# Kernel tuning notes

Measured on AMD Instinct MI355X. Metric: run time of the kernel, lower is better.

The kernel has to match this reference:

```python
import jax, jax.numpy as jnp
import numpy as np

BS, SEQ, D_MODEL = 4, 1024, 4096
N_Q_HEADS, N_KV_HEADS, D_K, D_V = 32, 8, 128, 128
ROPE_BASE = 10000.0


def _rotate_half(x):
    x1, x2 = jnp.split(x, 2, axis=-1)
    return jnp.concatenate([-x2, x1], axis=-1)


def _apply_rope(x, pos0):
    # x: [bs, heads, seq, d]; positions pos0 .. pos0+seq-1
    d = x.shape[-1]
    seq = x.shape[2]
    inv_freq = 1.0 / (ROPE_BASE ** (jnp.arange(0, d, 2, dtype=jnp.float32) / d))  # [d/2]
    pos = (pos0 + jnp.arange(seq)).astype(jnp.float32)  # [seq]
    ang = pos[:, None] * inv_freq[None, :]  # [seq, d/2]
    cos = jnp.concatenate([jnp.cos(ang), jnp.cos(ang)], axis=-1)  # [seq, d]
    sin = jnp.concatenate([jnp.sin(ang), jnp.sin(ang)], axis=-1)
    return x * cos[None, None] + _rotate_half(x) * sin[None, None]


def setup_inputs() -> dict:
    key = jax.random.key(0)
    ks = jax.random.split(key, 8)
    w_scale = 0.02  # keep logits in a sane range (original uses raw normal init)
    return {
        "query": jax.random.normal(ks[0], (BS, SEQ, D_MODEL), dtype=jnp.float32),
        "key": jax.random.normal(ks[1], (BS, SEQ, D_MODEL), dtype=jnp.float32),
        "value": jax.random.normal(ks[2], (BS, SEQ, D_MODEL), dtype=jnp.float32),
        "mask": jnp.zeros((BS, SEQ, SEQ), dtype=jnp.float32),
        "wq": jax.random.normal(ks[3], (D_MODEL, N_Q_HEADS * D_K), dtype=jnp.float32) * w_scale,
        "wk": jax.random.normal(ks[4], (D_MODEL, N_KV_HEADS * D_K), dtype=jnp.float32) * w_scale,
        "wv": jax.random.normal(ks[5], (D_MODEL, N_KV_HEADS * D_V), dtype=jnp.float32) * w_scale,
        "wo": jax.random.normal(ks[6], (N_Q_HEADS * D_V, D_MODEL), dtype=jnp.float32) * w_scale,
        "curr_seq_pos": 0,
    }


def reference(query, key, value, mask, wq, wk, wv, wo, curr_seq_pos):
    bs, sq, _ = query.shape
    n_groups = N_Q_HEADS // N_KV_HEADS
    # projections -> [bs, heads, seq, d]
    q = (query @ wq).reshape(bs, sq, N_Q_HEADS, D_K).transpose((0, 2, 1, 3))
    sk = key.shape[1]
    k = (key @ wk).reshape(bs, sk, N_KV_HEADS, 1, D_K)
    k = jnp.repeat(k, n_groups, axis=3).reshape(bs, sk, N_Q_HEADS, D_K).transpose((0, 2, 1, 3))
    v = (value @ wv).reshape(bs, sk, N_KV_HEADS, 1, D_V)
    v = jnp.repeat(v, n_groups, axis=3).reshape(bs, sk, N_Q_HEADS, D_V).transpose((0, 2, 1, 3))
    scale = jnp.sqrt(jnp.float32(D_K))
    q = _apply_rope(q, curr_seq_pos)
    k = _apply_rope(k, curr_seq_pos)
    # [bs, h, sq, sk]
    raw = jnp.einsum("bhqd,bhkd->bhqk", q, k) / scale
    masked = raw + mask[:bs, None, curr_seq_pos:curr_seq_pos + sq, :sk]
    attn = jax.nn.softmax(masked, axis=-1)
    out = jnp.einsum("bhqk,bhkd->bhqd", attn, v)
    out = out.transpose((0, 2, 1, 3)).reshape(bs, sq, N_Q_HEADS * D_V)
    return out @ wo
```

## Files before the change

kernel.cpp:

```cpp
#include <hip/hip_runtime.h>


using ushort = unsigned short;
typedef __attribute__((ext_vector_type(8))) short short8;
typedef __attribute__((ext_vector_type(4))) short short4v;
typedef __attribute__((ext_vector_type(4))) float f32x4;
typedef __attribute__((ext_vector_type(4))) unsigned int uint4v;

__device__ __forceinline__ ushort f2bf(float x) {
  unsigned int u = __float_as_uint(x);
  u += 0x7FFFu + ((u >> 16) & 1u);
  return (ushort)(u >> 16);
}
__device__ __forceinline__ float bf2f(ushort h) {
  return __uint_as_float(((unsigned int)h) << 16);
}
__device__ __forceinline__ unsigned int cvt_pk_bf16(float lo, float hi) {
  unsigned int r;
  asm("v_cvt_pk_bf16_f32 %0, %1, %2" : "=v"(r) : "v"(lo), "v"(hi));
  return r;
}

__device__ __forceinline__ void async_copy16(const void* g, void* l) {
  __builtin_amdgcn_global_load_lds((const __attribute__((address_space(1))) void*)g,
                                   (__attribute__((address_space(3))) void*)l, 16, 0, 0);
}

__global__ __launch_bounds__(256)
void cvt_f32_bf16(const float* __restrict__ in, ushort* __restrict__ out, int n4) {
  const int i = blockIdx.x * 256 + threadIdx.x;
  if (i < n4) {
    const float4 f = ((const float4*)in)[i];
    short4v v;
    v[0] = (short)f2bf(f.x); v[1] = (short)f2bf(f.y);
    v[2] = (short)f2bf(f.z); v[3] = (short)f2bf(f.w);
    ((short4v*)out)[i] = v;
  }
}

__global__ __launch_bounds__(256)
void transpose_cvt(const float* __restrict__ B, ushort* __restrict__ Bt, int N) {
  __shared__ ushort t[64][72];
  const int n0 = blockIdx.x * 64, k0 = blockIdx.y * 64;
  const int tid = threadIdx.x;
  const int r = tid >> 3, c8 = (tid & 7) * 8;
#pragma unroll
  for (int p = 0; p < 2; p++) {
    const float* src = B + (size_t)(k0 + r + p * 32) * N + n0 + c8;
    const float4 f0 = *(const float4*)src;
    const float4 f1 = *(const float4*)(src + 4);
    ushort* d = &t[r + p * 32][c8];
    d[0] = f2bf(f0.x); d[1] = f2bf(f0.y); d[2] = f2bf(f0.z); d[3] = f2bf(f0.w);
    d[4] = f2bf(f1.x); d[5] = f2bf(f1.y); d[6] = f2bf(f1.z); d[7] = f2bf(f1.w);
  }
  __syncthreads();
#pragma unroll
  for (int p = 0; p < 2; p++) {
    const int n = r + p * 32;
    short8 o;
#pragma unroll
    for (int j = 0; j < 8; j++) o[j] = (short)t[c8 + j][n];
    *(short8*)(Bt + (size_t)(n0 + n) * 4096 + k0 + c8) = o;
  }
}

template <int MODE, bool AF32>
__global__ __launch_bounds__(256, 2)
void gemm_bt(const float* __restrict__ Af, const float* __restrict__ A2f,
             const ushort* __restrict__ Abf, const ushort* __restrict__ Bt,
             ushort* __restrict__ C, ushort* __restrict__ C2,
             float* __restrict__ Cf, const int* __restrict__ posp,
             int N, float scale) {
  constexpr int K = 4096;
  __shared__ alignas(16) ushort As[2][128 * 32];
  __shared__ alignas(16) ushort Bs[2][128 * 32];
  const int tid = threadIdx.x;
  const int wave = tid >> 6, lane = tid & 63;
  const int quad = lane >> 4, l16 = lane & 15;
  const int m0 = blockIdx.y * 128, n0 = blockIdx.x * 128;
  const int wm = (wave & 1) * 64, wn2 = (wave >> 1) * 32;

  const size_t aoff = (size_t)(m0 + wave * 16 + (lane >> 2)) * K + (lane & 3) * 8;
  const float* gAf = nullptr;
  const ushort* gAb = nullptr;
  if constexpr (AF32) {
    const float* Ause = Af;
    if constexpr (MODE == 4) {
      if (n0 >= 1024) Ause = A2f;
    }
    gAf = Ause + aoff;
  } else {
    gAb = Abf + aoff;
  }
  const ushort* gB = Bt + (size_t)(n0 + wave * 16 + (lane >> 2)) * K + (lane & 3) * 8;
  const int woff = wave * 512;
  constexpr size_t rstep = (size_t)64 * K;

  f32x4 acc[4][4] = {};

  if constexpr (AF32) {
    const float4 a0 = *(const float4*)(gAf);
    const float4 a1 = *(const float4*)(gAf + 4);
    const float4 b0 = *(const float4*)(gAf + rstep);
    const float4 b1 = *(const float4*)(gAf + rstep + 4);
    uint4v v0, v1;
    v0[0] = cvt_pk_bf16(a0.x, a0.y); v0[1] = cvt_pk_bf16(a0.z, a0.w);
    v0[2] = cvt_pk_bf16(a1.x, a1.y); v0[3] = cvt_pk_bf16(a1.z, a1.w);
    v1[0] = cvt_pk_bf16(b0.x, b0.y); v1[1] = cvt_pk_bf16(b0.z, b0.w);
    v1[2] = cvt_pk_bf16(b1.x, b1.y); v1[3] = cvt_pk_bf16(b1.z, b1.w);
    *(uint4v*)(As[0] + woff + lane * 8) = v0;
    *(uint4v*)(As[0] + 2048 + woff + lane * 8) = v1;
  } else {
    async_copy16(gAb, As[0] + woff);
    async_copy16(gAb + rstep, As[0] + 2048 + woff);
  }
  async_copy16(gB, Bs[0] + woff);
  async_copy16(gB + rstep, Bs[0] + 2048 + woff);

  for (int kt = 0; kt < K; kt += 32) {
    const int cur = (kt >> 5) & 1;
    const int nxt = cur ^ 1;
    const bool pf = (kt + 32) < K;
    __syncthreads();

    float4 a0, a1, b0, b1;
    if constexpr (AF32) {
      if (pf) {
        a0 = *(const float4*)(gAf + kt + 32);
        a1 = *(const float4*)(gAf + kt + 36);
        b0 = *(const float4*)(gAf + rstep + kt + 32);
        b1 = *(const float4*)(gAf + rstep + kt + 36);
      }
    } else {
      if (pf) {
        async_copy16(gAb + kt + 32, As[nxt] + woff);
        async_copy16(gAb + rstep + kt + 32, As[nxt] + 2048 + woff);
      }
    }
    if (pf) {
      async_copy16(gB + kt + 32, Bs[nxt] + woff);
      async_copy16(gB + rstep + kt + 32, Bs[nxt] + 2048 + woff);
    }

    short8 af[4], bfrag[4];
#pragma unroll
    for (int i = 0; i < 4; i++) {
      af[i] = *(const short8*)(As[cur] + (wm + i * 16 + l16) * 32 + quad * 8);
      bfrag[i] = *(const short8*)(
          Bs[cur] + (wn2 + (i & 1) * 16 + (i >> 1) * 64 + l16) * 32 + quad * 8);
    }
    __builtin_amdgcn_s_setprio(1);
#pragma unroll
    for (int i = 0; i < 4; i++)
#pragma unroll
      for (int j = 0; j < 4; j++)
        acc[i][j] = __builtin_amdgcn_mfma_f32_16x16x32_bf16(af[i], bfrag[j],
                                                            acc[i][j], 0, 0, 0);
    __builtin_amdgcn_s_setprio(0);

    if constexpr (AF32) {
      if (pf) {
        uint4v v0, v1;
        v0[0] = cvt_pk_bf16(a0.x, a0.y); v0[1] = cvt_pk_bf16(a0.z, a0.w);
        v0[2] = cvt_pk_bf16(a1.x, a1.y); v0[3] = cvt_pk_bf16(a1.z, a1.w);
        v1[0] = cvt_pk_bf16(b0.x, b0.y); v1[1] = cvt_pk_bf16(b0.z, b0.w);
        v1[2] = cvt_pk_bf16(b1.x, b1.y); v1[3] = cvt_pk_bf16(b1.z, b1.w);
        *(uint4v*)(As[nxt] + woff + lane * 8) = v0;
        *(uint4v*)(As[nxt] + 2048 + woff + lane * 8) = v1;
      }
    }
  }

  if constexpr (MODE == 0) {
#pragma unroll
    for (int i = 0; i < 4; i++)
#pragma unroll
      for (int j = 0; j < 4; j++) {
        const int n = n0 + wn2 + (j & 1) * 16 + (j >> 1) * 64 + l16;
        const int mb = m0 + wm + i * 16 + quad * 4;
#pragma unroll
        for (int r = 0; r < 4; r++)
          Cf[(size_t)(mb + r) * N + n] = acc[i][j][r] * scale;
      }
  } else {
    const bool kv_v = (MODE == 4) && (n0 >= 1024);
    if (!kv_v) {
      const int pos0 = posp[0];
      const int h = (MODE == 1) ? (n0 >> 7) : (n0 >> 7);
      const int NH = (MODE == 1) ? 32 : 8;
      constexpr float lgbase = -0.20762050593045983f;
      float invf[2];
      invf[0] = exp2f((float)(wn2 + l16) * lgbase);
      invf[1] = exp2f((float)(wn2 + 16 + l16) * lgbase);
#pragma unroll
      for (int i = 0; i < 4; i++) {
#pragma unroll
        for (int r = 0; r < 4; r++) {
          const int m = m0 + wm + i * 16 + quad * 4 + r;
          const int s = m & 1023, bb = m >> 10;
          const float p = (float)(s + pos0);
          ushort* row = C + (((size_t)bb * NH + h) * 1024 + s) * 128;
#pragma unroll
          for (int jj = 0; jj < 2; jj++) {
            float sn, cs;
            sincosf(p * invf[jj], &sn, &cs);
            const float x1 = acc[i][jj][r] * scale;
            const float x2 = acc[i][jj + 2][r] * scale;
            const int dlo = wn2 + jj * 16 + l16;
            row[dlo] = f2bf(x1 * cs - x2 * sn);
            row[dlo + 64] = f2bf(x2 * cs + x1 * sn);
          }
        }
      }
    } else {
      const int hh = (n0 - 1024) >> 7;
#pragma unroll
      for (int i = 0; i < 4; i++)
#pragma unroll
        for (int j = 0; j < 4; j++) {
          const int d = wn2 + (j & 1) * 16 + (j >> 1) * 64 + l16;
          const int mb = m0 + wm + i * 16 + quad * 4;
#pragma unroll
          for (int r = 0; r < 4; r++) {
            const int m = mb + r;
            const int bb = m >> 10, s = m & 1023;
            C2[(((size_t)bb * 8 + hh) * 128 + d) * 1024 + s] = f2bf(acc[i][j][r]);
          }
        }
    }
  }
}

__global__ __launch_bounds__(256, 2)
void attn_kernel(const ushort* __restrict__ Qh, const ushort* __restrict__ Kh,
                 const ushort* __restrict__ Vt, const ushort* __restrict__ Mk,
                 ushort* __restrict__ Oh) {
  __shared__ alignas(16) ushort smem[36864];
  ushort* const Ks0 = smem;
  ushort* const Ks1 = smem + 8192;
  ushort* const Vs0 = smem + 16384;
  ushort* const Vs1 = smem + 24576;
  ushort* const Ps = smem + 32768;
  ushort* const Qtmp = smem + 16384;

  int bid = (blockIdx.z * 32 + blockIdx.y) * 16 + blockIdx.x;
  bid = (bid & 7) * 256 + (bid >> 3);
  const int b = bid >> 9, h = (bid >> 4) & 31;
  const int q0 = (bid & 15) * 64;
  const int hkv = h >> 2;
  const int tid = threadIdx.x;
  const int wave = tid >> 6, lane = tid & 63;
  const int quad = lane >> 4, l16 = lane & 15;
  const int vr = lane >> 3;
  const int vkc = (lane & 7) ^ (vr & 7);

  const ushort* Qg = Qh + (((size_t)b * 32 + h) * 1024 + q0) * 128;
  const ushort* Kg = Kh + ((size_t)b * 8 + hkv) * (size_t)(1024 * 128);
  const ushort* Vg = Vt + ((size_t)b * 8 + hkv) * (size_t)(128 * 1024);
  const ushort* Mg = Mk + ((size_t)b * 1024 + q0) * 1024;

#pragma unroll
  for (int c = 0; c < 4; c++) {
    const int i = wave * 4 + c;
    const int row = i * 4 + quad;
    const int kc = l16 ^ (c * 4 + quad);
    async_copy16(Qg + (size_t)row * 128 + kc * 8, Qtmp + i * 512);
  }
#pragma unroll
  for (int c = 0; c < 4; c++) {
    const int i = wave * 4 + c;
    const int row = i * 4 + quad;
    const int kc = l16 ^ (c * 4 + quad);
    async_copy16(Kg + (size_t)row * 128 + kc * 8, Ks0 + i * 512);
  }
  __asm__ volatile("s_waitcnt vmcnt(0)" ::: "memory");
  short8 qreg[4];
#pragma unroll
  for (int ks = 0; ks < 4; ks++)
    qreg[ks] = *(const short8*)(Qtmp + (size_t)(wave * 16 + l16) * 128 +
                                (((ks * 4 + quad) ^ l16) * 8));
  __syncthreads();
#pragma unroll
  for (int c = 0; c < 4; c++) {
    const int i = wave * 4 + c;
    async_copy16(Vg + (size_t)(i * 8 + vr) * 1024 + vkc * 8, Vs0 + i * 512);
  }

  float m_i[4], l_p[4];
#pragma unroll
  for (int r = 0; r < 4; r++) { m_i[r] = -1e30f; l_p[r] = 0.0f; }
  f32x4 acc[8] = {};

  ushort* const PW = Ps + wave * 1024;

  for (int kt = 0; kt < 1024; kt += 64) {
    const int it = kt >> 6;
    ushort* const Kc = (it & 1) ? Ks1 : Ks0;
    ushort* const Vc = (it & 1) ? Vs1 : Vs0;
    ushort* const Kn = (it & 1) ? Ks0 : Ks1;
    ushort* const Vn = (it & 1) ? Vs0 : Vs1;
    __syncthreads();

    ushort mr[4][4];
#pragma unroll
    for (int nt = 0; nt < 4; nt++)
#pragma unroll
      for (int r = 0; r < 4; r++)
        mr[nt][r] = Mg[(size_t)(wave * 16 + quad * 4 + r) * 1024 +
                       kt + nt * 16 + l16];

    f32x4 s[4] = {};
    __builtin_amdgcn_s_setprio(1);
#pragma unroll
    for (int ks = 0; ks < 4; ks++) {
      const int ko = ((ks * 4 + quad) ^ l16) * 8;
#pragma unroll
      for (int nt = 0; nt < 4; nt++) {
        const short8 bk = *(const short8*)(Kc + (size_t)(nt * 16 + l16) * 128 + ko);
        s[nt] = __builtin_amdgcn_mfma_f32_16x16x32_bf16(qreg[ks], bk, s[nt], 0, 0, 0);
      }
    }
    __builtin_amdgcn_s_setprio(0);

    if (kt < 960) {
#pragma unroll
      for (int c = 0; c < 4; c++) {
        const int i = wave * 4 + c;
        const int row = i * 4 + quad;
        const int kc = l16 ^ (c * 4 + quad);
        async_copy16(Kg + (size_t)(kt + 64 + row) * 128 + kc * 8, Kn + i * 512);
      }
#pragma unroll
      for (int c = 0; c < 4; c++) {
        const int i = wave * 4 + c;
        async_copy16(Vg + (size_t)(i * 8 + vr) * 1024 + kt + 64 + vkc * 8, Vn + i * 512);
      }
    }

#pragma unroll
    for (int nt = 0; nt < 4; nt++)
#pragma unroll
      for (int r = 0; r < 4; r++) s[nt][r] += bf2f(mr[nt][r]);

    float mx[4];
    int need = 0;
#pragma unroll
    for (int r = 0; r < 4; r++) {
      float v = fmaxf(fmaxf(s[0][r], s[1][r]), fmaxf(s[2][r], s[3][r]));
#pragma unroll
      for (int off = 1; off < 16; off <<= 1) v = fmaxf(v, __shfl_xor(v, off));
      mx[r] = v;
      need |= (v > m_i[r] + 8.0f) ? 1 : 0;
    }
    if (__any(need)) {
#pragma unroll
      for (int r = 0; r < 4; r++) {
        const float mnew = fmaxf(m_i[r], mx[r]);
        const float al = __expf(m_i[r] - mnew);
        m_i[r] = mnew;
        l_p[r] *= al;
#pragma unroll
        for (int dt = 0; dt < 8; dt++) acc[dt][r] *= al;
      }
    }

#pragma unroll
    for (int r = 0; r < 4; r++) {
      const int prow = quad * 4 + r;
      const int key8 = ((prow >> 1) & 7) * 8;
      const float p0 = __expf(s[0][r] - m_i[r]);
      const float p1 = __expf(s[1][r] - m_i[r]);
      const float p2 = __expf(s[2][r] - m_i[r]);
      const float p3 = __expf(s[3][r] - m_i[r]);
      l_p[r] += (p0 + p1) + (p2 + p3);
      const unsigned int u01 = cvt_pk_bf16(p0, p1);
      const unsigned int u23 = cvt_pk_bf16(p2, p3);
      ushort* row = PW + prow * 64;
      row[l16 ^ key8] = (ushort)u01;
      row[(16 + l16) ^ key8] = (ushort)(u01 >> 16);
      row[(32 + l16) ^ key8] = (ushort)u23;
      row[(48 + l16) ^ key8] = (ushort)(u23 >> 16);
    }
    __asm__ volatile("s_waitcnt lgkmcnt(0)" ::: "memory");

    __builtin_amdgcn_s_setprio(1);
#pragma unroll
    for (int kk = 0; kk < 2; kk++) {
      const int pslot = ((kk * 4 + quad) ^ (l16 >> 1)) * 8;
      const short8 ap = *(const short8*)(PW + (size_t)l16 * 64 + pslot);
#pragma unroll
      for (int dt = 0; dt < 8; dt++) {
        const int vo = ((kk * 4 + quad) ^ (l16 & 7)) * 8;
        const short8 bv = *(const short8*)(Vc + (size_t)(dt * 16 + l16) * 64 + vo);
        acc[dt] = __builtin_amdgcn_mfma_f32_16x16x32_bf16(ap, bv, acc[dt], 0, 0, 0);
      }
    }
    __builtin_amdgcn_s_setprio(0);
  }

  ushort* Og = Oh + ((size_t)b * 1024 + q0 + wave * 16) * 4096 + h * 128;
#pragma unroll
  for (int r = 0; r < 4; r++) {
    float l = l_p[r];
#pragma unroll
    for (int off = 1; off < 16; off <<= 1) l += __shfl_xor(l, off);
    const float inv = 1.0f / l;
#pragma unroll
    for (int dt = 0; dt < 8; dt++)
      Og[(size_t)(quad * 4 + r) * 4096 + dt * 16 + l16] = f2bf(acc[dt][r] * inv);
  }
}

extern "C" void kernel_launch(void* const* d_in, const int* in_sizes, int n_in,
                              void* d_out, int out_size, void* d_ws, size_t ws_size,
                              hipStream_t stream) {
  (void)in_sizes; (void)n_in; (void)out_size; (void)ws_size;
  const float* query = (const float*)d_in[0];
  const float* key = (const float*)d_in[1];
  const float* value = (const float*)d_in[2];
  const float* mask = (const float*)d_in[3];
  const float* wq = (const float*)d_in[4];
  const float* wk = (const float*)d_in[5];
  const float* wv = (const float*)d_in[6];
  const float* wo = (const float*)d_in[7];
  const int* pos = (const int*)d_in[8];
  float* out = (float*)d_out;

  char* ws = (char*)d_ws;
  const size_t MB = 1024 * 1024;
  ushort* qb = (ushort*)(ws + 0 * MB);
  ushort* Khb = (ushort*)(ws + 0 * MB);
  ushort* Vtb = (ushort*)(ws + 8 * MB);
  ushort* wqT = (ushort*)(ws + 32 * MB);
  ushort* wkvT = (ushort*)(ws + 32 * MB);
  ushort* Ohb = (ushort*)(ws + 32 * MB);
  ushort* Qhb = (ushort*)(ws + 64 * MB);
  ushort* woT = (ushort*)(ws + 64 * MB);
  ushort* mbf = (ushort*)(ws + 96 * MB);

  dim3 blk(256);
  cvt_f32_bf16<<<dim3(4096), blk, 0, stream>>>(mask, mbf, 1048576);
  cvt_f32_bf16<<<dim3(16384), blk, 0, stream>>>(query, qb, 4194304);

  transpose_cvt<<<dim3(64, 64), blk, 0, stream>>>(wq, wqT, 4096);
  gemm_bt<1, false><<<dim3(32, 32), blk, 0, stream>>>(
      nullptr, nullptr, qb, wqT, Qhb, nullptr, nullptr, pos, 4096,
      0.08838834764831845f);

  transpose_cvt<<<dim3(16, 64), blk, 0, stream>>>(wk, wkvT, 1024);
  transpose_cvt<<<dim3(16, 64), blk, 0, stream>>>(wv, wkvT + (size_t)1024 * 4096, 1024);
  gemm_bt<4, true><<<dim3(16, 32), blk, 0, stream>>>(
      key, value, nullptr, wkvT, Khb, Vtb, nullptr, pos, 2048, 1.0f);

  attn_kernel<<<dim3(16, 32, 4), blk, 0, stream>>>(Qhb, Khb, Vtb, mbf, Ohb);

  transpose_cvt<<<dim3(64, 64), blk, 0, stream>>>(wo, woT, 4096);
  gemm_bt<0, false><<<dim3(32, 32), blk, 0, stream>>>(
      nullptr, nullptr, Ohb, woT, nullptr, nullptr, out, pos, 4096, 1.0f);
}
```

Before: 932.7 us.

## Add 256x256-tile 8-wave GEMM with quadrant pipelining for Q and output projections

Introduces a new GEMM kernel with 256x256 block tiles, 512 threads, a 128KB LDS double buffer with XOR swizzle, and async global-to-LDS loads. Loads for the next k-tile are staged in quarters that interleave with MFMA work on four sub-quadrants, using s_setprio and explicit waitcnt/barriers. Both the 4096x4096x4096 Q projection (with fused RoPE) and the output projection now use it in place of the 128x128 kernel. This raises reuse per LDS byte and overlaps memory with compute, at the cost of a grid of only 256 blocks and heavy register and LDS use that limits occupancy.

```diff
diff --git a/kernel.cpp b/kernel.cpp
--- a/kernel.cpp
+++ b/kernel.cpp
@@ -61,6 +61,185 @@
 #pragma unroll
     for (int j = 0; j < 8; j++) o[j] = (short)t[c8 + j][n];
     *(short8*)(Bt + (size_t)(n0 + n) * 4096 + k0 + c8) = o;
+  }
+}
+
+template <int MQ>
+__device__ __forceinline__ void read_afrag(const ushort* Ab, int arbase,
+                                           const int (&kslot)[2], short8 (&af)[2][2]) {
+#pragma unroll
+  for (int f = 0; f < 2; f++)
+#pragma unroll
+    for (int kk = 0; kk < 2; kk++)
+      af[f][kk] = *(const short8*)(Ab + MQ * 8192 + arbase + f * 1024 + kslot[kk]);
+}
+template <int NQ>
+__device__ __forceinline__ void read_bfrag(const ushort* Bb, int brbase,
+                                           const int (&kslot)[2], short8 (&bg)[4][2]) {
+#pragma unroll
+  for (int g = 0; g < 4; g++)
+#pragma unroll
+    for (int kk = 0; kk < 2; kk++)
+      bg[g][kk] = *(const short8*)(Bb + NQ * 8192 + brbase + (g & 1) * 1024 +
+                                   (g >> 1) * 4096 + kslot[kk]);
+}
+__device__ __forceinline__ void mma_quad(short8 (&af)[2][2], short8 (&bg)[4][2],
+                                         f32x4 (&q)[2][4]) {
+#pragma unroll
+  for (int f = 0; f < 2; f++)
+#pragma unroll
+    for (int g = 0; g < 4; g++)
+#pragma unroll
+      for (int kk = 0; kk < 2; kk++)
+        q[f][g] = __builtin_amdgcn_mfma_f32_16x16x32_bf16(af[f][kk], bg[g][kk],
+                                                          q[f][g], 0, 0, 0);
+}
+
+template <int MODE>
+__global__ __launch_bounds__(512, 2)
+void gemm256(const ushort* __restrict__ A, const ushort* __restrict__ Bt,
+             ushort* __restrict__ C, float* __restrict__ Cf,
+             const int* __restrict__ posp, int N, float scale) {
+  constexpr int K = 4096, NT = 64;
+  __shared__ alignas(16) ushort lds[65536];
+  const int tid = threadIdx.x;
+  const int wave = tid >> 6, lane = tid & 63;
+  const int quad = lane >> 4, l16 = lane & 15;
+  const int wr = wave & 3, wc = wave >> 2;
+  const int m0 = blockIdx.y * 256, n0 = blockIdx.x * 256;
+
+  const int srow = tid >> 3, schunk = (tid & 7) ^ ((tid >> 3) & 7);
+  const ushort* gA = A + (size_t)(m0 + srow) * K + schunk * 8;
+  const ushort* gB = Bt + (size_t)(n0 + srow) * K + schunk * 8;
+  ushort* const stbase = lds + wave * 512;
+
+  const int sw = l16 & 7;
+  const int kslot[2] = {(quad ^ sw) * 8, ((4 + quad) ^ sw) * 8};
+  const int arbase = (wr * 32 + l16) * 64;
+  const int brbase = (wc * 32 + l16) * 64;
+
+  short8 af[2][2], bg[4][2];
+  f32x4 acc[2][2][2][4] = {};
+
+  auto STAGE = [&](int bufo, int isB, int half, int t) {
+    const ushort* src = (isB ? gB : gA) + (size_t)(half * 128) * K + t * 64;
+    ushort* dst = stbase + bufo + isB * 16384 + half * 8192;
+    async_copy16(src, dst);
+    async_copy16(src + (size_t)64 * K, dst + 4096);
+  };
+
+  STAGE(0, 0, 0, 0);
+  STAGE(0, 1, 0, 0);
+  STAGE(0, 1, 1, 0);
+  STAGE(0, 0, 1, 0);
+  __asm__ volatile("s_waitcnt vmcnt(4)" ::: "memory");
+  __builtin_amdgcn_s_barrier();
+
+  for (int t = 0; t < NT; ++t) {
+    const int bo = (t & 1) << 15;
+    const int bn = bo ^ 32768;
+    const bool pf = (t + 1) < NT;
+    const ushort* Ab = lds + bo;
+    const ushort* Bb = lds + bo + 16384;
+
+    read_afrag<0>(Ab, arbase, kslot, af);
+    read_bfrag<0>(Bb, brbase, kslot, bg);
+    if (pf) STAGE(bn, 0, 0, t + 1);
+    __asm__ volatile("s_waitcnt lgkmcnt(8)" ::: "memory");
+    __builtin_amdgcn_s_barrier();
+    __asm__ volatile("s_waitcnt lgkmcnt(0)" ::: "memory");
+    __builtin_amdgcn_sched_barrier(0);
+    __builtin_amdgcn_s_setprio(1);
+    mma_quad(af, bg, acc[0][0]);
+    __builtin_amdgcn_s_setprio(0);
+    if (pf) {
+      __asm__ volatile("s_waitcnt vmcnt(2)" ::: "memory");
+    } else {
+      __asm__ volatile("s_waitcnt vmcnt(0)" ::: "memory");
+    }
+    __builtin_amdgcn_s_barrier();
+
+    read_afrag<1>(Ab, arbase, kslot, af);
+    if (pf) STAGE(bn, 1, 0, t + 1);
+    __builtin_amdgcn_s_barrier();
+    __asm__ volatile("s_waitcnt lgkmcnt(0)" ::: "memory");
+    __builtin_amdgcn_sched_barrier(0);
+    __builtin_amdgcn_s_setprio(1);
+    mma_quad(af, bg, acc[1][0]);
+    __builtin_amdgcn_s_setprio(0);
+    __builtin_amdgcn_s_barrier();
+
+    read_bfrag<1>(Bb, brbase, kslot, bg);
+    if (pf) STAGE(bn, 1, 1, t + 1);
+    __builtin_amdgcn_s_barrier();
+    __asm__ volatile("s_waitcnt lgkmcnt(0)" ::: "memory");
+    __builtin_amdgcn_sched_barrier(0);
+    __builtin_amdgcn_s_setprio(1);
+    mma_quad(af, bg, acc[1][1]);
+    __builtin_amdgcn_s_setprio(0);
+    __builtin_amdgcn_s_barrier();
+
+    read_afrag<0>(Ab, arbase, kslot, af);
+    if (pf) STAGE(bn, 0, 1, t + 1);
+    __builtin_amdgcn_s_barrier();
+    __asm__ volatile("s_waitcnt lgkmcnt(0)" ::: "memory");
+    __builtin_amdgcn_sched_barrier(0);
+    __builtin_amdgcn_s_setprio(1);
+    mma_quad(af, bg, acc[0][1]);
+    __builtin_amdgcn_s_setprio(0);
+    if (pf) {
+      __asm__ volatile("s_waitcnt vmcnt(4)" ::: "memory");
+    }
+    __builtin_amdgcn_s_barrier();
+  }
+
+  if constexpr (MODE == 0) {
+#pragma unroll
+    for (int Mq = 0; Mq < 2; Mq++)
+#pragma unroll
+      for (int Nq = 0; Nq < 2; Nq++)
+#pragma unroll
+        for (int f = 0; f < 2; f++)
+#pragma unroll
+          for (int g = 0; g < 4; g++) {
+            const int m = m0 + Mq * 128 + wr * 32 + f * 16 + quad * 4;
+            const int n = n0 + Nq * 128 + wc * 32 + (g & 1) * 16 +
+                          (g >> 1) * 64 + l16;
+#pragma unroll
+            for (int rr = 0; rr < 4; rr++)
+              Cf[(size_t)(m + rr) * N + n] = acc[Mq][Nq][f][g][rr] * scale;
+          }
+  } else {
+    const int pos0 = posp[0];
+    constexpr float lgbase = -0.20762050593045983f;
+    float invf[2];
+    invf[0] = exp2f((float)(wc * 32 + l16) * lgbase);
+    invf[1] = exp2f((float)(wc * 32 + 16 + l16) * lgbase);
+#pragma unroll
+    for (int Mq = 0; Mq < 2; Mq++)
+#pragma unroll
+      for (int f = 0; f < 2; f++)
+#pragma unroll
+        for (int rr = 0; rr < 4; rr++) {
+          const int m = m0 + Mq * 128 + wr * 32 + f * 16 + quad * 4 + rr;
+          const int s = m & 1023, bb = m >> 10;
+          const float p = (float)(s + pos0);
+#pragma unroll
+          for (int Nq = 0; Nq < 2; Nq++) {
+            const int h = blockIdx.x * 2 + Nq;
+            ushort* row = C + (((size_t)bb * 32 + h) * 1024 + s) * 128;
+#pragma unroll
+            for (int g = 0; g < 2; g++) {
+              float sn, cs;
+              sincosf(p * invf[g], &sn, &cs);
+              const float x1 = acc[Mq][Nq][f][g][rr] * scale;
+              const float x2 = acc[Mq][Nq][f][g + 2][rr] * scale;
+              const int dlo = wc * 32 + g * 16 + l16;
+              row[dlo] = f2bf(x1 * cs - x2 * sn);
+              row[dlo + 64] = f2bf(x2 * cs + x1 * sn);
+            }
+          }
+        }
   }
 }
 
@@ -186,7 +365,7 @@
     const bool kv_v = (MODE == 4) && (n0 >= 1024);
     if (!kv_v) {
       const int pos0 = posp[0];
-      const int h = (MODE == 1) ? (n0 >> 7) : (n0 >> 7);
+      const int h = n0 >> 7;
       const int NH = (MODE == 1) ? 32 : 8;
       constexpr float lgbase = -0.20762050593045983f;
       float invf[2];
@@ -443,9 +622,8 @@
   cvt_f32_bf16<<<dim3(16384), blk, 0, stream>>>(query, qb, 4194304);
 
   transpose_cvt<<<dim3(64, 64), blk, 0, stream>>>(wq, wqT, 4096);
-  gemm_bt<1, false><<<dim3(32, 32), blk, 0, stream>>>(
-      nullptr, nullptr, qb, wqT, Qhb, nullptr, nullptr, pos, 4096,
-      0.08838834764831845f);
+  gemm256<1><<<dim3(16, 16), dim3(512), 0, stream>>>(
+      qb, wqT, Qhb, nullptr, pos, 4096, 0.08838834764831845f);
 
   transpose_cvt<<<dim3(16, 64), blk, 0, stream>>>(wk, wkvT, 1024);
   transpose_cvt<<<dim3(16, 64), blk, 0, stream>>>(wv, wkvT + (size_t)1024 * 4096, 1024);
@@ -455,6 +633,6 @@
   attn_kernel<<<dim3(16, 32, 4), blk, 0, stream>>>(Qhb, Khb, Vtb, mbf, Ohb);
 
   transpose_cvt<<<dim3(64, 64), blk, 0, stream>>>(wo, woT, 4096);
-  gemm_bt<0, false><<<dim3(32, 32), blk, 0, stream>>>(
-      nullptr, nullptr, Ohb, woT, nullptr, nullptr, out, pos, 4096, 1.0f);
-}
+  gemm256<0><<<dim3(16, 16), dim3(512), 0, stream>>>(
+      Ohb, woT, nullptr, out, pos, 4096, 1.0f);
+}
```

Result: no change. 919.6 us (-1.4%).
